# Optimization experiments

Measured on AMD Instinct MI355X. Metric: run time of the kernel, lower is better.

The kernel has to match this reference:

```python
import jax, jax.numpy as jnp
import numpy as np

T = 1.0  # temperature (default in original forward)


def setup_inputs() -> dict:
    key = jax.random.key(0)
    k1, k2 = jax.random.split(key)
    N, M, D = 65536, 512, 256
    z = jax.random.normal(k1, (N, D), dtype=jnp.float32)
    e = jax.random.normal(k2, (M, D), dtype=jnp.float32)
    log_sigma = jnp.zeros((1,), dtype=jnp.float32)  # init_log_sigma = 0.0
    return {"z": z, "e": e, "log_sigma": log_sigma}


def reference(z, e, log_sigma):
    N, z_dim = z.shape
    M = e.shape[0]
    # pad N up to a multiple of M (zeros), then view as [B, M, z_dim]
    N_pad = ((N + M - 1) // M) * M
    z = jnp.pad(z, ((0, N_pad - N), (0, 0)))
    zb = z.reshape(-1, M, z_dim)  # [B, M, D]
    # squared euclidean distance via GEMM form: ||z||^2 + ||e||^2 - 2 z.e -> [B, M, M]
    dist = (
        jnp.sum(zb * zb, axis=-1)[:, :, None]
        + jnp.sum(e * e, axis=-1)[None, None, :]
        - 2.0 * jnp.einsum("bmd,kd->bmk", zb, e)
    )
    alpha = -1.0 / (2.0 * jnp.exp(log_sigma[0]) ** 2)
    # logsumexp over the z-block dim (axis=1), mean over codebook dim (axis=1 after reduce)
    loss = -jnp.mean(T * jax.nn.logsumexp(alpha * dist / T, axis=1), axis=1)  # [B]
    loss = loss + 0.5 * z_dim * (2.0 * log_sigma[0] - 1.0) + jnp.log(jnp.float32(M))
    return jnp.mean(loss)
```

## Files before the change

### kernel.cpp

```cpp
#include <hip/hip_runtime.h>
#include <stdint.h>
#include <math.h>

typedef __attribute__((ext_vector_type(8))) short short8;
typedef __attribute__((ext_vector_type(16))) float f32x16;

#define DEVI static __device__ __forceinline__

constexpr int D = 256;
constexpr float LOG2E = 1.4426950408889634f;
constexpr float LN2   = 0.6931471805599453f;

constexpr size_t WS_EIMG  = 0;
constexpr size_t WS_ETERM = 262144;
constexpr size_t WS_WMAX  = 264192;
constexpr size_t WS_WSUM  = WS_WMAX + 2097152;
constexpr size_t WS_PART  = WS_WSUM + 2097152;

DEVI unsigned int f2bf(float f) {
  unsigned int u = __float_as_uint(f);
  return (u + 0x7fffu + ((u >> 16) & 1u)) >> 16;
}
DEVI float shflx(float v, int m) { return __shfl_xor(v, m, 64); }

__global__ void prep_e(const float* __restrict__ e, const float* __restrict__ lsp,
                       char* __restrict__ eimg, float* __restrict__ eterm) {
  const int et = blockIdx.x, t = threadIdx.x;
  const int c = t >> 3, o = t & 7;
  const int gc = et * 32 + c;
  const float a = __expf(-2.0f * lsp[0]);
  const float sab = a * LOG2E;
  const float* s = e + (size_t)gc * D + o * 32;
  float sq = 0.0f;
  unsigned int w[16];
#pragma unroll
  for (int i = 0; i < 8; ++i) {
    float4 x = *(const float4*)(s + i * 4);
    sq += x.x * x.x + x.y * x.y + x.z * x.z + x.w * x.w;
    w[2 * i]     = f2bf(sab * x.x) | (f2bf(sab * x.y) << 16);
    w[2 * i + 1] = f2bf(sab * x.z) | (f2bf(sab * x.w) << 16);
  }
  sq += shflx(sq, 1); sq += shflx(sq, 2); sq += shflx(sq, 4);
  char* base = eimg + (size_t)et * 16384;
#pragma unroll
  for (int i = 0; i < 4; ++i) {
    int g = o * 4 + i;
    int phys = (g >> 1) * 1024 + (g & 1) * 512 + c * 16;
    uint4 pk; pk.x = w[4 * i]; pk.y = w[4 * i + 1];
    pk.z = w[4 * i + 2]; pk.w = w[4 * i + 3];
    *(uint4*)(base + phys) = pk;
  }
  if (o == 0) eterm[gc] = -0.5f * a * sq;
}

__global__ __launch_bounds__(512, 4)
void lse_main(const float* __restrict__ z, const char* __restrict__ eimg,
              const float* __restrict__ lsp, float* __restrict__ wmax,
              float* __restrict__ wsum) {
  __shared__ char  zbuf[32768];
  __shared__ float ztm[64];

  const int tid = threadIdx.x;
  const int wid = tid >> 6, lane = tid & 63;
  const int l31 = lane & 31;
  const int hi  = lane >> 5;
  const int bx = blockIdx.x;
  const float a = __expf(-2.0f * lsp[0]);
  const float ztf = -0.5f * a * LOG2E;

  {
    const int row = tid >> 3, o = tid & 7;
    const float* src = z + ((size_t)bx * 64 + row) * D + o * 32;
    float sq = 0.0f;
#pragma unroll
    for (int i = 0; i < 4; ++i) {
      float4 x0 = *(const float4*)(src + i * 8);
      float4 x1 = *(const float4*)(src + i * 8 + 4);
      sq += x0.x * x0.x + x0.y * x0.y + x0.z * x0.z + x0.w * x0.w +
            x1.x * x1.x + x1.y * x1.y + x1.z * x1.z + x1.w * x1.w;
      uint4 pk;
      pk.x = f2bf(x0.x) | (f2bf(x0.y) << 16);
      pk.y = f2bf(x0.z) | (f2bf(x0.w) << 16);
      pk.z = f2bf(x1.x) | (f2bf(x1.y) << 16);
      pk.w = f2bf(x1.z) | (f2bf(x1.w) << 16);
      const int g = o * 4 + i;
      *(uint4*)(zbuf + row * 512 + ((g ^ (row & 31)) * 16)) = pk;
    }
    sq += shflx(sq, 1); sq += shflx(sq, 2); sq += shflx(sq, 4);
    if (o == 0) ztm[row] = ztf * sq;
  }
  __syncthreads();

  f32x16 acc00, acc01, acc10, acc11;
#pragma unroll
  for (int i = 0; i < 16; ++i) { acc00[i] = 0.f; acc01[i] = 0.f;
                                 acc10[i] = 0.f; acc11[i] = 0.f; }
  const char* eb0 = eimg + (size_t)(2 * wid) * 16384 + lane * 16;
  const char* ab0 = zbuf + l31 * 512;
  const char* ab1 = zbuf + (32 + l31) * 512;
#pragma unroll
  for (int s = 0; s < 16; ++s) {
    const int g = 2 * s + hi;
    const int key = (g ^ l31) * 16;
    short8 A0 = *(const short8*)(ab0 + key);
    short8 A1 = *(const short8*)(ab1 + key);
    short8 B0 = *(const short8*)(eb0 + s * 1024);
    short8 B1 = *(const short8*)(eb0 + 16384 + s * 1024);
    acc00 = __builtin_amdgcn_mfma_f32_32x32x16_bf16(A0, B0, acc00, 0, 0, 0);
    acc01 = __builtin_amdgcn_mfma_f32_32x32x16_bf16(A0, B1, acc01, 0, 0, 0);
    acc10 = __builtin_amdgcn_mfma_f32_32x32x16_bf16(A1, B0, acc10, 0, 0, 0);
    acc11 = __builtin_amdgcn_mfma_f32_32x32x16_bf16(A1, B1, acc11, 0, 0, 0);
  }

#pragma unroll
  for (int r = 0; r < 16; ++r) {
    const int rr = (r & 3) + 8 * (r >> 2) + 4 * hi;
    const float zt0 = ztm[rr];
    const float zt1 = ztm[32 + rr];
    acc00[r] += zt0; acc01[r] += zt0;
    acc10[r] += zt1; acc11[r] += zt1;
  }
  float mx0 = -1e30f, mx1 = -1e30f;
#pragma unroll
  for (int r = 0; r < 16; ++r) {
    mx0 = fmaxf(mx0, fmaxf(acc00[r], acc10[r]));
    mx1 = fmaxf(mx1, fmaxf(acc01[r], acc11[r]));
  }
  mx0 = fmaxf(mx0, shflx(mx0, 32));
  mx1 = fmaxf(mx1, shflx(mx1, 32));
  float sm0 = 0.f, sm1 = 0.f;
#pragma unroll
  for (int r = 0; r < 16; ++r) {
    sm0 += exp2f(acc00[r] - mx0) + exp2f(acc10[r] - mx0);
    sm1 += exp2f(acc01[r] - mx1) + exp2f(acc11[r] - mx1);
  }
  sm0 += shflx(sm0, 32);
  sm1 += shflx(sm1, 32);
  if (hi == 0) {
    const int col = wid * 64 + l31;
    wmax[(size_t)bx * 512 + col] = mx0;
    wsum[(size_t)bx * 512 + col] = sm0;
    wmax[(size_t)bx * 512 + 32 + col] = mx1;
    wsum[(size_t)bx * 512 + 32 + col] = sm1;
  }
}

__global__ void merge_b(const float* __restrict__ wmax, const float* __restrict__ wsum,
                        const float* __restrict__ eterm, float* __restrict__ partial) {
  __shared__ float sh[512];
  const int b = blockIdx.x, t = threadIdx.x;
  float m[8];
  float nm = -1e30f;
#pragma unroll
  for (int i = 0; i < 8; ++i) {
    m[i] = wmax[(size_t)(8 * b + i) * 512 + t];
    nm = fmaxf(nm, m[i]);
  }
  float s = 0.0f;
#pragma unroll
  for (int i = 0; i < 8; ++i)
    s += wsum[(size_t)(8 * b + i) * 512 + t] * exp2f(m[i] - nm);
  sh[t] = LN2 * (nm + log2f(s)) + eterm[t];
  __syncthreads();
  for (int st = 256; st > 0; st >>= 1) {
    if (t < st) sh[t] += sh[t + st];
    __syncthreads();
  }
  if (t == 0) partial[b] = sh[0];
}

__global__ void final_k(const float* __restrict__ partial,
                        const float* __restrict__ lsp, float* __restrict__ out) {
  __shared__ float sh[128];
  const int t = threadIdx.x;
  sh[t] = partial[t];
  __syncthreads();
  for (int st = 64; st > 0; st >>= 1) {
    if (t < st) sh[t] += sh[t + st];
    __syncthreads();
  }
  if (t == 0) {
    float ls = lsp[0];
    out[0] = -sh[0] / 65536.0f + 128.0f * (2.0f * ls - 1.0f) + logf(512.0f);
  }
}

extern "C" void kernel_launch(void* const* d_in, const int* in_sizes, int n_in,
                              void* d_out, int out_size, void* d_ws, size_t ws_size,
                              hipStream_t stream) {
  const float* z   = (const float*)d_in[0];
  const float* e   = (const float*)d_in[1];
  const float* lsp = (const float*)d_in[2];
  float* out = (float*)d_out;
  char* ws = (char*)d_ws;
  char*  eimg    = ws + WS_EIMG;
  float* eterm   = (float*)(ws + WS_ETERM);
  float* wmax    = (float*)(ws + WS_WMAX);
  float* wsum    = (float*)(ws + WS_WSUM);
  float* partial = (float*)(ws + WS_PART);

  prep_e<<<dim3(16), dim3(256), 0, stream>>>(e, lsp, eimg, eterm);
  lse_main<<<dim3(1024), dim3(512), 0, stream>>>(z, eimg, lsp, wmax, wsum);
  merge_b<<<dim3(128), dim3(512), 0, stream>>>(wmax, wsum, eterm, partial);
  final_k<<<dim3(1), dim3(128), 0, stream>>>(partial, lsp, out);
}
```

Baseline: 45.03 us.

## Split codebook across two blocks per row tile and prefetch B fragments

The main kernel now launches twice as many blocks, each covering 64 z rows against half of the codebook. Each wave computes a 64x32 tile with two MFMA accumulators instead of four. B fragments from the E image are prefetched four steps ahead in registers, z conversion uses the packed v_cvt_pk_bf16_f32 instruction, and the max/sum reductions use independent partial accumulators. Splitting the codebook means every z tile is loaded and converted twice (once per half), in exchange for more parallelism and lower register pressure per wave.

New measurement: 46.78 us. 3.9% more time.

```diff
diff --git a/kernel.cpp b/kernel.cpp
--- a/kernel.cpp
+++ b/kernel.cpp
@@ -21,6 +21,12 @@
   unsigned int u = __float_as_uint(f);
   return (u + 0x7fffu + ((u >> 16) & 1u)) >> 16;
 }
+DEVI unsigned int cvtpk(float lo, float hi) {
+  unsigned int r;
+  asm("v_cvt_pk_bf16_f32 %0, %1, %2" : "=v"(r) : "v"(lo), "v"(hi));
+  return r;
+}
+DEVI float d4(float4 x) { return x.x*x.x + x.y*x.y + x.z*x.z + x.w*x.w; }
 DEVI float shflx(float v, int m) { return __shfl_xor(v, m, 64); }
 
 __global__ void prep_e(const float* __restrict__ e, const float* __restrict__ lsp,
@@ -36,7 +42,7 @@
 #pragma unroll
   for (int i = 0; i < 8; ++i) {
     float4 x = *(const float4*)(s + i * 4);
-    sq += x.x * x.x + x.y * x.y + x.z * x.z + x.w * x.w;
+    sq += d4(x);
     w[2 * i]     = f2bf(sab * x.x) | (f2bf(sab * x.y) << 16);
     w[2 * i + 1] = f2bf(sab * x.z) | (f2bf(sab * x.w) << 16);
   }
@@ -65,83 +71,95 @@
   const int l31 = lane & 31;
   const int hi  = lane >> 5;
   const int bx = blockIdx.x;
+  const int rowblk = bx >> 1, half = bx & 1;
   const float a = __expf(-2.0f * lsp[0]);
   const float ztf = -0.5f * a * LOG2E;
 
   {
-    const int row = tid >> 3, o = tid & 7;
-    const float* src = z + ((size_t)bx * 64 + row) * D + o * 32;
-    float sq = 0.0f;
-#pragma unroll
-    for (int i = 0; i < 4; ++i) {
-      float4 x0 = *(const float4*)(src + i * 8);
-      float4 x1 = *(const float4*)(src + i * 8 + 4);
-      sq += x0.x * x0.x + x0.y * x0.y + x0.z * x0.z + x0.w * x0.w +
-            x1.x * x1.x + x1.y * x1.y + x1.z * x1.z + x1.w * x1.w;
-      uint4 pk;
-      pk.x = f2bf(x0.x) | (f2bf(x0.y) << 16);
-      pk.y = f2bf(x0.z) | (f2bf(x0.w) << 16);
-      pk.z = f2bf(x1.x) | (f2bf(x1.y) << 16);
-      pk.w = f2bf(x1.z) | (f2bf(x1.w) << 16);
-      const int g = o * 4 + i;
-      *(uint4*)(zbuf + row * 512 + ((g ^ (row & 31)) * 16)) = pk;
-    }
-    sq += shflx(sq, 1); sq += shflx(sq, 2); sq += shflx(sq, 4);
-    if (o == 0) ztm[row] = ztf * sq;
+    const int srow = tid >> 4;
+    const int gp = (tid & 15) * 2;
+    const float* p0 = z + ((size_t)rowblk * 64 + srow) * D + gp * 8;
+    const float* p1 = p0 + (size_t)32 * D;
+    float4 u0 = *(const float4*)(p0),     u1 = *(const float4*)(p0 + 4);
+    float4 u2 = *(const float4*)(p0 + 8), u3 = *(const float4*)(p0 + 12);
+    float4 w0 = *(const float4*)(p1),     w1 = *(const float4*)(p1 + 4);
+    float4 w2 = *(const float4*)(p1 + 8), w3 = *(const float4*)(p1 + 12);
+    float squ = d4(u0) + d4(u1) + d4(u2) + d4(u3);
+    float sqw = d4(w0) + d4(w1) + d4(w2) + d4(w3);
+    squ += shflx(squ, 1); squ += shflx(squ, 2);
+    squ += shflx(squ, 4); squ += shflx(squ, 8);
+    sqw += shflx(sqw, 1); sqw += shflx(sqw, 2);
+    sqw += shflx(sqw, 4); sqw += shflx(sqw, 8);
+    uint4 a0, a1, b0, b1;
+    a0.x = cvtpk(u0.x, u0.y); a0.y = cvtpk(u0.z, u0.w);
+    a0.z = cvtpk(u1.x, u1.y); a0.w = cvtpk(u1.z, u1.w);
+    a1.x = cvtpk(u2.x, u2.y); a1.y = cvtpk(u2.z, u2.w);
+    a1.z = cvtpk(u3.x, u3.y); a1.w = cvtpk(u3.z, u3.w);
+    b0.x = cvtpk(w0.x, w0.y); b0.y = cvtpk(w0.z, w0.w);
+    b0.z = cvtpk(w1.x, w1.y); b0.w = cvtpk(w1.z, w1.w);
+    b1.x = cvtpk(w2.x, w2.y); b1.y = cvtpk(w2.z, w2.w);
+    b1.z = cvtpk(w3.x, w3.y); b1.w = cvtpk(w3.z, w3.w);
+    char* rb = zbuf + srow * 512;
+    *(uint4*)(rb + ((gp ^ srow) * 16))             = a0;
+    *(uint4*)(rb + (((gp + 1) ^ srow) * 16))       = a1;
+    *(uint4*)(rb + 16384 + ((gp ^ srow) * 16))     = b0;
+    *(uint4*)(rb + 16384 + (((gp + 1) ^ srow) * 16)) = b1;
+    if ((tid & 15) == 0) { ztm[srow] = ztf * squ; ztm[32 + srow] = ztf * sqw; }
   }
   __syncthreads();
 
-  f32x16 acc00, acc01, acc10, acc11;
-#pragma unroll
-  for (int i = 0; i < 16; ++i) { acc00[i] = 0.f; acc01[i] = 0.f;
-                                 acc10[i] = 0.f; acc11[i] = 0.f; }
-  const char* eb0 = eimg + (size_t)(2 * wid) * 16384 + lane * 16;
-  const char* ab0 = zbuf + l31 * 512;
-  const char* ab1 = zbuf + (32 + l31) * 512;
+  const char* bp = eimg + (size_t)(half * 8 + wid) * 16384 + (size_t)lane * 16;
+  short8 Bq[4];
+#pragma unroll
+  for (int i = 0; i < 4; ++i) Bq[i] = *(const short8*)(bp + i * 1024);
+
+  f32x16 acc0, acc1;
+#pragma unroll
+  for (int i = 0; i < 16; ++i) { acc0[i] = 0.f; acc1[i] = 0.f; }
+  const int C0 = l31 * 512 + ((hi * 16) ^ (l31 * 16));
 #pragma unroll
   for (int s = 0; s < 16; ++s) {
-    const int g = 2 * s + hi;
-    const int key = (g ^ l31) * 16;
-    short8 A0 = *(const short8*)(ab0 + key);
-    short8 A1 = *(const short8*)(ab1 + key);
-    short8 B0 = *(const short8*)(eb0 + s * 1024);
-    short8 B1 = *(const short8*)(eb0 + 16384 + s * 1024);
-    acc00 = __builtin_amdgcn_mfma_f32_32x32x16_bf16(A0, B0, acc00, 0, 0, 0);
-    acc01 = __builtin_amdgcn_mfma_f32_32x32x16_bf16(A0, B1, acc01, 0, 0, 0);
-    acc10 = __builtin_amdgcn_mfma_f32_32x32x16_bf16(A1, B0, acc10, 0, 0, 0);
-    acc11 = __builtin_amdgcn_mfma_f32_32x32x16_bf16(A1, B1, acc11, 0, 0, 0);
-  }
-
+    short8 Bc = Bq[s & 3];
+    if (s + 4 < 16) Bq[s & 3] = *(const short8*)(bp + (s + 4) * 1024);
+    const int slot = C0 ^ (s * 32);
+    short8 A0 = *(const short8*)(zbuf + slot);
+    short8 A1 = *(const short8*)(zbuf + slot + 16384);
+    acc0 = __builtin_amdgcn_mfma_f32_32x32x16_bf16(A0, Bc, acc0, 0, 0, 0);
+    acc1 = __builtin_amdgcn_mfma_f32_32x32x16_bf16(A1, Bc, acc1, 0, 0, 0);
+  }
+
+  float4 zt0[4], zt1[4];
+#pragma unroll
+  for (int j = 0; j < 4; ++j) {
+    zt0[j] = *(const float4*)&ztm[8 * j + 4 * hi];
+    zt1[j] = *(const float4*)&ztm[32 + 8 * j + 4 * hi];
+  }
+  float v[32];
 #pragma unroll
   for (int r = 0; r < 16; ++r) {
-    const int rr = (r & 3) + 8 * (r >> 2) + 4 * hi;
-    const float zt0 = ztm[rr];
-    const float zt1 = ztm[32 + rr];
-    acc00[r] += zt0; acc01[r] += zt0;
-    acc10[r] += zt1; acc11[r] += zt1;
-  }
-  float mx0 = -1e30f, mx1 = -1e30f;
-#pragma unroll
-  for (int r = 0; r < 16; ++r) {
-    mx0 = fmaxf(mx0, fmaxf(acc00[r], acc10[r]));
-    mx1 = fmaxf(mx1, fmaxf(acc01[r], acc11[r]));
-  }
-  mx0 = fmaxf(mx0, shflx(mx0, 32));
-  mx1 = fmaxf(mx1, shflx(mx1, 32));
-  float sm0 = 0.f, sm1 = 0.f;
-#pragma unroll
-  for (int r = 0; r < 16; ++r) {
-    sm0 += exp2f(acc00[r] - mx0) + exp2f(acc10[r] - mx0);
-    sm1 += exp2f(acc01[r] - mx1) + exp2f(acc11[r] - mx1);
-  }
-  sm0 += shflx(sm0, 32);
-  sm1 += shflx(sm1, 32);
+    v[r]      = acc0[r] + ((const float*)&zt0[r >> 2])[r & 3];
+    v[16 + r] = acc1[r] + ((const float*)&zt1[r >> 2])[r & 3];
+  }
+  float m0 = v[0], m1 = v[1], m2 = v[2], m3 = v[3];
+#pragma unroll
+  for (int i = 4; i < 32; i += 4) {
+    m0 = fmaxf(m0, v[i]);     m1 = fmaxf(m1, v[i + 1]);
+    m2 = fmaxf(m2, v[i + 2]); m3 = fmaxf(m3, v[i + 3]);
+  }
+  float mx = fmaxf(fmaxf(m0, m1), fmaxf(m2, m3));
+  mx = fmaxf(mx, shflx(mx, 32));
+  float s0 = 0.f, s1 = 0.f, s2 = 0.f, s3 = 0.f;
+#pragma unroll
+  for (int i = 0; i < 32; i += 4) {
+    s0 += exp2f(v[i] - mx);     s1 += exp2f(v[i + 1] - mx);
+    s2 += exp2f(v[i + 2] - mx); s3 += exp2f(v[i + 3] - mx);
+  }
+  float sm = (s0 + s1) + (s2 + s3);
+  sm += shflx(sm, 32);
   if (hi == 0) {
-    const int col = wid * 64 + l31;
-    wmax[(size_t)bx * 512 + col] = mx0;
-    wsum[(size_t)bx * 512 + col] = sm0;
-    wmax[(size_t)bx * 512 + 32 + col] = mx1;
-    wsum[(size_t)bx * 512 + 32 + col] = sm1;
+    const int col = half * 256 + wid * 32 + l31;
+    wmax[(size_t)rowblk * 512 + col] = mx;
+    wsum[(size_t)rowblk * 512 + col] = sm;
   }
 }
 
@@ -200,7 +218,7 @@
   float* partial = (float*)(ws + WS_PART);
 
   prep_e<<<dim3(16), dim3(256), 0, stream>>>(e, lsp, eimg, eterm);
-  lse_main<<<dim3(1024), dim3(512), 0, stream>>>(z, eimg, lsp, wmax, wsum);
+  lse_main<<<dim3(2048), dim3(512), 0, stream>>>(z, eimg, lsp, wmax, wsum);
   merge_b<<<dim3(128), dim3(512), 0, stream>>>(wmax, wsum, eterm, partial);
   final_k<<<dim3(1), dim3(128), 0, stream>>>(partial, lsp, out);
 }
```
